# Performance work log

Hardware: AMD Instinct MI355X
Metric: run time of the kernel (lower is better)

The kernel has to match this reference:

```python
import jax, jax.numpy as jnp
import numpy as np

D_MODEL = 128
D_EDGE = 64


def setup_inputs() -> dict:
    key = jax.random.key(0)
    ks = jax.random.split(key, 12)
    B, N, E = 4, 50000, 600000
    x = jax.random.normal(ks[0], (B, N, D_MODEL), dtype=jnp.float32)
    edge_index = jax.random.randint(ks[1], (2, E), 0, N, dtype=jnp.int64)
    e_emb = jax.random.normal(ks[2], (E, D_EDGE), dtype=jnp.float32)
    batch_index = jax.random.randint(ks[3], (E,), 0, B, dtype=jnp.int64)
    s = 1.0 / np.sqrt(D_MODEL)
    se = 1.0 / np.sqrt(D_EDGE)
    Wq = jax.random.normal(ks[4], (D_MODEL, D_MODEL), dtype=jnp.float32) * s
    bq = jnp.zeros((D_MODEL,), dtype=jnp.float32)
    Wk = jax.random.normal(ks[5], (D_MODEL, D_MODEL), dtype=jnp.float32) * s
    bk = jnp.zeros((D_MODEL,), dtype=jnp.float32)
    Wv = jax.random.normal(ks[6], (D_MODEL, D_MODEL), dtype=jnp.float32) * s
    bv = jnp.zeros((D_MODEL,), dtype=jnp.float32)
    Wew = jax.random.normal(ks[7], (D_EDGE, D_MODEL), dtype=jnp.float32) * se
    bew = jnp.zeros((D_MODEL,), dtype=jnp.float32)
    Wev = jax.random.normal(ks[8], (D_EDGE, D_MODEL), dtype=jnp.float32) * se
    bev = jnp.zeros((D_MODEL,), dtype=jnp.float32)
    Wa = jax.random.normal(ks[9], (D_MODEL, 1), dtype=jnp.float32) * s
    return {"x": x, "edge_index": edge_index, "e_emb": e_emb,
            "batch_index": batch_index, "n_heads": 8,
            "Wq": Wq, "bq": bq, "Wk": Wk, "bk": bk, "Wv": Wv, "bv": bv,
            "Wew": Wew, "bew": bew, "Wev": Wev, "bev": bev, "Wa": Wa}


def reference(x, edge_index, e_emb, batch_index, n_heads,
              Wq, bq, Wk, bk, Wv, bv, Wew, bew, Wev, bev, Wa):
    B, N, d = x.shape
    d_h = d // n_heads
    Q = x @ Wq + bq          # [B, N, d]
    K = x @ Wk + bk
    V = x @ Wv + bv
    Ew = e_emb @ Wew + bew   # [E, d]
    Ev = e_emb @ Wev + bev
    src, dst = edge_index[0], edge_index[1]
    q_src = Q[batch_index, src, :]   # [E, d] gathers
    k_dst = K[batch_index, dst, :]
    v_dst = V[batch_index, dst, :]
    att_raw = q_src + k_dst + Ew
    att_logit = (att_raw @ Wa)[:, 0] / np.sqrt(d_h).astype(np.float32)
    att_exp = jnp.exp(att_logit)     # [E]
    group = batch_index * N + dst
    att_sum = jax.ops.segment_sum(att_exp, group, num_segments=B * N)
    alpha = att_exp / (att_sum[group] + 1e-9)
    msg = alpha[:, None] * (v_dst + Ev)          # [E, d]
    group_src = batch_index * N + src
    out_flat = jax.ops.segment_sum(msg, group_src, num_segments=B * N)
    return out_flat.reshape(B, N, d)
```

## Files before the change

### kernel.cpp

```cpp
#include <hip/hip_runtime.h>

#define DM 128
#define DE 64

static constexpr int kB = 4;
static constexpr int kN = 50000;
static constexpr int kE = 600000;
static constexpr int kNodes = kB * kN;

static constexpr size_t OFF_V    = 0;
static constexpr size_t OFF_T    = OFF_V + (size_t)kNodes * DM;
static constexpr size_t OFF_QA   = OFF_T + (size_t)kNodes * DE;
static constexpr size_t OFF_KA   = OFF_QA + kNodes;
static constexpr size_t OFF_ASUM = OFF_KA + kNodes;
static constexpr size_t OFF_CNT  = OFF_ASUM + kNodes;
static constexpr size_t OFF_AEXP = OFF_CNT + kNodes;
static constexpr size_t OFF_OFFS = OFF_AEXP + kE;
static constexpr size_t OFF_POS  = OFF_OFFS + kNodes;
static constexpr size_t OFF_BSUM = OFF_POS + kE;
static constexpr size_t OFF_BPRE = OFF_BSUM + 1024;
static constexpr size_t OFF_REC  = OFF_BPRE + 1024;
static constexpr size_t OFF_WQA  = OFF_REC + (size_t)kE * 4;
static constexpr size_t OFF_WKA  = OFF_WQA + DM;
static constexpr size_t OFF_WEWA = OFF_WKA + DM;
static constexpr size_t OFF_CB   = OFF_WEWA + DE;

static constexpr int kScanBlocks = (kNodes + 255) / 256;

__global__ void k0_combine(const float* __restrict__ Wq, const float* __restrict__ Wk,
                           const float* __restrict__ Wew, const float* __restrict__ Wa,
                           const float* __restrict__ bq, const float* __restrict__ bk,
                           const float* __restrict__ bew, float* __restrict__ ws) {
  int t = threadIdx.x;
  if (t < DM) {
    float a = 0.f;
    for (int j = 0; j < DM; ++j) a += Wq[t * DM + j] * Wa[j];
    ws[OFF_WQA + t] = a;
  } else if (t < 2 * DM) {
    int i = t - DM;
    float a = 0.f;
    for (int j = 0; j < DM; ++j) a += Wk[i * DM + j] * Wa[j];
    ws[OFF_WKA + i] = a;
  } else if (t < 2 * DM + DE) {
    int i = t - 2 * DM;
    float a = 0.f;
    for (int j = 0; j < DM; ++j) a += Wew[i * DM + j] * Wa[j];
    ws[OFF_WEWA + i] = a;
  }
  if (t == 0) {
    float a = 0.f;
    for (int j = 0; j < DM; ++j) a += (bq[j] + bk[j] + bew[j]) * Wa[j];
    ws[OFF_CB] = a;
  }
}

__global__ __launch_bounds__(256) void k1_node(const float* __restrict__ x,
                                               const float* __restrict__ Wv,
                                               const float* __restrict__ bv,
                                               float* __restrict__ ws) {
  __shared__ float xs[64][132];
  __shared__ float wvs[32][132];
  const int t = threadIdx.x;
  const int row0 = blockIdx.x * 64;

  const float4* xg = (const float4*)(x + (size_t)row0 * DM);
  #pragma unroll
  for (int i = 0; i < 8; ++i) {
    int idx = t + i * 256;
    int r = idx >> 5, c = (idx & 31) * 4;
    *(float4*)&xs[r][c] = xg[idx];
  }
  __syncthreads();

  if (t < 128) {
    const int r = t & 63;
    const float* wvec = (t < 64) ? (ws + OFF_WQA) : (ws + OFF_WKA);
    float a = 0.f;
    for (int k = 0; k < DM; k += 4) {
      a += xs[r][k] * wvec[k] + xs[r][k + 1] * wvec[k + 1] +
           xs[r][k + 2] * wvec[k + 2] + xs[r][k + 3] * wvec[k + 3];
    }
    float* dstp = (t < 64) ? (ws + OFF_QA) : (ws + OFF_KA);
    dstp[row0 + r] = a;
  }

  const int tx = t & 15, ty = t >> 4;
  const int j0 = tx * 8, r0 = ty * 4;
  float acc[4][8];
  #pragma unroll
  for (int i = 0; i < 4; ++i)
    #pragma unroll
    for (int j = 0; j < 8; ++j) acc[i][j] = 0.f;

  for (int kc = 0; kc < 4; ++kc) {
    __syncthreads();
    const float4* wg = (const float4*)(Wv + (size_t)kc * 32 * DM);
    #pragma unroll
    for (int i = 0; i < 4; ++i) {
      int idx = t + i * 256;
      int r = idx >> 5, c = (idx & 31) * 4;
      *(float4*)&wvs[r][c] = wg[idx];
    }
    __syncthreads();
    const int kb = kc * 32;
    #pragma unroll
    for (int kk = 0; kk < 32; kk += 4) {
      float xv[4][4];
      #pragma unroll
      for (int i = 0; i < 4; ++i) {
        float4 tmp = *(const float4*)&xs[r0 + i][kb + kk];
        xv[i][0] = tmp.x; xv[i][1] = tmp.y; xv[i][2] = tmp.z; xv[i][3] = tmp.w;
      }
      #pragma unroll
      for (int d = 0; d < 4; ++d) {
        float4 w0 = *(const float4*)&wvs[kk + d][j0];
        float4 w1 = *(const float4*)&wvs[kk + d][j0 + 4];
        float wj[8] = {w0.x, w0.y, w0.z, w0.w, w1.x, w1.y, w1.z, w1.w};
        #pragma unroll
        for (int i = 0; i < 4; ++i)
          #pragma unroll
          for (int j = 0; j < 8; ++j) acc[i][j] += xv[i][d] * wj[j];
      }
    }
  }

  const float4 bv0 = *(const float4*)&bv[j0];
  const float4 bv1 = *(const float4*)&bv[j0 + 4];
  float* Vp = ws + OFF_V + (size_t)row0 * DM;
  #pragma unroll
  for (int i = 0; i < 4; ++i) {
    float4 o0 = make_float4(acc[i][0] + bv0.x, acc[i][1] + bv0.y,
                            acc[i][2] + bv0.z, acc[i][3] + bv0.w);
    float4 o1 = make_float4(acc[i][4] + bv1.x, acc[i][5] + bv1.y,
                            acc[i][6] + bv1.z, acc[i][7] + bv1.w);
    *(float4*)&Vp[(size_t)(r0 + i) * DM + j0] = o0;
    *(float4*)&Vp[(size_t)(r0 + i) * DM + j0 + 4] = o1;
  }
}

__global__ __launch_bounds__(256) void k2_edge1(const int* __restrict__ ei,
                                                const int* __restrict__ bidx,
                                                const float* __restrict__ eemb,
                                                float* __restrict__ ws) {
  __shared__ float wewa_s[DE];
  __shared__ float cb_s;
  int t = threadIdx.x;
  if (t < DE) wewa_s[t] = ws[OFF_WEWA + t];
  if (t == DE) cb_s = ws[OFF_CB];
  __syncthreads();
  int e = blockIdx.x * 256 + t;
  if (e >= kE) return;
  int s = ei[e];
  int d = ei[kE + e];
  int b = bidx[e];
  const float4* emb = (const float4*)(eemb + (size_t)e * DE);
  float a = 0.f;
  #pragma unroll
  for (int i = 0; i < 16; ++i) {
    float4 v = emb[i];
    a += v.x * wewa_s[i * 4] + v.y * wewa_s[i * 4 + 1] +
         v.z * wewa_s[i * 4 + 2] + v.w * wewa_s[i * 4 + 3];
  }
  float logit = (ws[OFF_QA + b * kN + s] + ws[OFF_KA + b * kN + d] + a + cb_s) * 0.25f;
  float ex = __expf(logit);
  ws[OFF_AEXP + e] = ex;
  unsafeAtomicAdd(&ws[OFF_ASUM + b * kN + d], ex);
  int* wsi = (int*)ws;
  int gs = b * kN + s;
  wsi[OFF_POS + e] = atomicAdd(&wsi[OFF_CNT + gs], 1);
}

__global__ __launch_bounds__(256) void k_scan1(float* __restrict__ ws) {
  __shared__ int sh[256];
  int* wsi = (int*)ws;
  const int tid = threadIdx.x;
  const int i = blockIdx.x * 256 + tid;
  int v = (i < kNodes) ? wsi[OFF_CNT + i] : 0;
  int acc = v;
  sh[tid] = acc;
  __syncthreads();
  #pragma unroll
  for (int ofs = 1; ofs < 256; ofs <<= 1) {
    int add = (tid >= ofs) ? sh[tid - ofs] : 0;
    __syncthreads();
    acc += add;
    sh[tid] = acc;
    __syncthreads();
  }
  if (i < kNodes) wsi[OFF_OFFS + i] = acc - v;
  if (tid == 255) wsi[OFF_BSUM + blockIdx.x] = acc;
}

__global__ __launch_bounds__(1024) void k_scan2(float* __restrict__ ws) {
  __shared__ int sh[1024];
  int* wsi = (int*)ws;
  const int tid = threadIdx.x;
  int v = (tid < kScanBlocks) ? wsi[OFF_BSUM + tid] : 0;
  int acc = v;
  sh[tid] = acc;
  __syncthreads();
  for (int ofs = 1; ofs < 1024; ofs <<= 1) {
    int add = (tid >= ofs) ? sh[tid - ofs] : 0;
    __syncthreads();
    acc += add;
    sh[tid] = acc;
    __syncthreads();
  }
  wsi[OFF_BPRE + tid] = acc - v;
}

__global__ __launch_bounds__(256) void k_fill(const int* __restrict__ ei,
                                              const int* __restrict__ bidx,
                                              float* __restrict__ ws) {
  int e = blockIdx.x * 256 + threadIdx.x;
  if (e >= kE) return;
  int s = ei[e];
  int d = ei[kE + e];
  int b = bidx[e];
  int gs = b * kN + s;
  int gd = b * kN + d;
  const int* wsi = (const int*)ws;
  float alpha = ws[OFF_AEXP + e] / (ws[OFF_ASUM + gd] + 1e-9f);
  int p = wsi[OFF_OFFS + gs] + wsi[OFF_BPRE + (gs >> 8)] + wsi[OFF_POS + e];
  float4 r;
  r.x = alpha;
  r.y = __int_as_float(gd);
  r.z = __int_as_float(e);
  r.w = 0.f;
  ((float4*)(ws + OFF_REC))[p] = r;
}

__global__ __launch_bounds__(256) void k3_gather(const float* __restrict__ eemb,
                                                 const float* __restrict__ bev,
                                                 float* __restrict__ ws,
                                                 float* __restrict__ out) {
  const int lane = threadIdx.x & 63;
  const int g = (blockIdx.x * 256 + threadIdx.x) >> 6;
  if (g >= kNodes) return;
  const int* wsi = (const int*)ws;
  const float* V = ws + OFF_V;
  float* T = ws + OFF_T;
  const float4* rec = (const float4*)(ws + OFF_REC);
  const float bev0 = bev[lane];
  const float bev1 = bev[64 + lane];

  const int start = wsi[OFF_OFFS + g] + wsi[OFF_BPRE + (g >> 8)];
  const int deg = wsi[OFF_CNT + g];
  float o0 = 0.f, o1 = 0.f, tac = 0.f, ss = 0.f;
  for (int base = 0; base < deg; base += 4) {
    const int rem = deg - base;
    const int c1 = (rem > 1) ? 1 : 0;
    const int c2 = (rem > 2) ? 2 : c1;
    const int c3 = (rem > 3) ? 3 : c2;
    float4 r0 = rec[start + base];
    float4 r1 = rec[start + base + c1];
    float4 r2 = rec[start + base + c2];
    float4 r3 = rec[start + base + c3];
    float a0 = r0.x;
    float a1 = (rem > 1) ? r1.x : 0.f;
    float a2 = (rem > 2) ? r2.x : 0.f;
    float a3 = (rem > 3) ? r3.x : 0.f;
    const size_t gd0 = (size_t)__float_as_int(r0.y) * DM;
    const size_t gd1 = (size_t)__float_as_int(r1.y) * DM;
    const size_t gd2 = (size_t)__float_as_int(r2.y) * DM;
    const size_t gd3 = (size_t)__float_as_int(r3.y) * DM;
    const size_t e0 = (size_t)__float_as_int(r0.z) * DE;
    const size_t e1 = (size_t)__float_as_int(r1.z) * DE;
    const size_t e2 = (size_t)__float_as_int(r2.z) * DE;
    const size_t e3 = (size_t)__float_as_int(r3.z) * DE;
    float v00 = V[gd0 + lane],      v01 = V[gd1 + lane];
    float v02 = V[gd2 + lane],      v03 = V[gd3 + lane];
    float v10 = V[gd0 + 64 + lane], v11 = V[gd1 + 64 + lane];
    float v12 = V[gd2 + 64 + lane], v13 = V[gd3 + 64 + lane];
    float m0 = eemb[e0 + lane],     m1 = eemb[e1 + lane];
    float m2 = eemb[e2 + lane],     m3 = eemb[e3 + lane];
    o0 += a0 * v00 + a1 * v01 + a2 * v02 + a3 * v03;
    o1 += a0 * v10 + a1 * v11 + a2 * v12 + a3 * v13;
    tac += a0 * m0 + a1 * m1 + a2 * m2 + a3 * m3;
    ss += a0 + a1 + a2 + a3;
  }
  out[(size_t)g * DM + lane] = o0 + ss * bev0;
  out[(size_t)g * DM + 64 + lane] = o1 + ss * bev1;
  T[(size_t)g * DE + lane] = tac;
}

__global__ __launch_bounds__(256) void k4_wev(const float* __restrict__ Wev,
                                              float* __restrict__ ws,
                                              float* __restrict__ out) {
  __shared__ float ts[64][68];
  __shared__ float wes[64][132];
  const int t = threadIdx.x;
  const int row0 = blockIdx.x * 64;
  const float* T = ws + OFF_T;

  const float4* tg = (const float4*)(T + (size_t)row0 * DE);
  #pragma unroll
  for (int i = 0; i < 4; ++i) {
    int idx = t + i * 256;
    int r = idx >> 4, c = (idx & 15) * 4;
    *(float4*)&ts[r][c] = tg[idx];
  }
  const float4* wg = (const float4*)Wev;
  #pragma unroll
  for (int i = 0; i < 8; ++i) {
    int idx = t + i * 256;
    int r = idx >> 5, c = (idx & 31) * 4;
    *(float4*)&wes[r][c] = wg[idx];
  }
  __syncthreads();

  const int tx = t & 15, ty = t >> 4;
  const int j0 = tx * 8, r0 = ty * 4;
  float acc[4][8];
  #pragma unroll
  for (int i = 0; i < 4; ++i)
    #pragma unroll
    for (int j = 0; j < 8; ++j) acc[i][j] = 0.f;

  #pragma unroll
  for (int kk = 0; kk < DE; kk += 4) {
    float xv[4][4];
    #pragma unroll
    for (int i = 0; i < 4; ++i) {
      float4 tmp = *(const float4*)&ts[r0 + i][kk];
      xv[i][0] = tmp.x; xv[i][1] = tmp.y; xv[i][2] = tmp.z; xv[i][3] = tmp.w;
    }
    #pragma unroll
    for (int d = 0; d < 4; ++d) {
      float4 w0 = *(const float4*)&wes[kk + d][j0];
      float4 w1 = *(const float4*)&wes[kk + d][j0 + 4];
      float wj[8] = {w0.x, w0.y, w0.z, w0.w, w1.x, w1.y, w1.z, w1.w};
      #pragma unroll
      for (int i = 0; i < 4; ++i)
        #pragma unroll
        for (int j = 0; j < 8; ++j) acc[i][j] += xv[i][d] * wj[j];
    }
  }

  #pragma unroll
  for (int i = 0; i < 4; ++i) {
    size_t g = (size_t)(row0 + r0 + i);
    float4 o0 = *(const float4*)&out[g * DM + j0];
    float4 o1 = *(const float4*)&out[g * DM + j0 + 4];
    o0.x += acc[i][0]; o0.y += acc[i][1]; o0.z += acc[i][2]; o0.w += acc[i][3];
    o1.x += acc[i][4]; o1.y += acc[i][5]; o1.z += acc[i][6]; o1.w += acc[i][7];
    *(float4*)&out[g * DM + j0] = o0;
    *(float4*)&out[g * DM + j0 + 4] = o1;
  }
}

extern "C" void kernel_launch(void* const* d_in, const int* in_sizes, int n_in,
                              void* d_out, int out_size, void* d_ws, size_t ws_size,
                              hipStream_t stream) {
  const float* x    = (const float*)d_in[0];
  const int*   ei   = (const int*)d_in[1];
  const float* eemb = (const float*)d_in[2];
  const int*   bidx = (const int*)d_in[3];
  const float* Wq  = (const float*)d_in[5];
  const float* bq  = (const float*)d_in[6];
  const float* Wk  = (const float*)d_in[7];
  const float* bk  = (const float*)d_in[8];
  const float* Wv  = (const float*)d_in[9];
  const float* bv  = (const float*)d_in[10];
  const float* Wew = (const float*)d_in[11];
  const float* bew = (const float*)d_in[12];
  const float* Wev = (const float*)d_in[13];
  const float* bev = (const float*)d_in[14];
  const float* Wa  = (const float*)d_in[15];
  float* ws  = (float*)d_ws;
  float* out = (float*)d_out;

  hipMemsetAsync(ws + OFF_ASUM, 0, (size_t)2 * kNodes * sizeof(float), stream);

  k0_combine<<<1, 320, 0, stream>>>(Wq, Wk, Wew, Wa, bq, bk, bew, ws);
  k1_node<<<kNodes / 64, 256, 0, stream>>>(x, Wv, bv, ws);
  k2_edge1<<<(kE + 255) / 256, 256, 0, stream>>>(ei, bidx, eemb, ws);
  k_scan1<<<kScanBlocks, 256, 0, stream>>>(ws);
  k_scan2<<<1, 1024, 0, stream>>>(ws);
  k_fill<<<(kE + 255) / 256, 256, 0, stream>>>(ei, bidx, ws);
  k3_gather<<<kNodes / 4, 256, 0, stream>>>(eemb, bev, ws, out);
  k4_wev<<<kNodes / 64, 256, 0, stream>>>(Wev, ws, out);
}
```

Before: 633.9 us.

## Compute V projection with split-bf16 MFMA instead of FP32 FMA tiles

Replaces the FP32 SIMT GEMM for V = x@Wv with bf16x3-style MFMA (hi*hi + hi*lo + lo*hi) on 128-row tiles with swizzled LDS layouts. A new pre-kernel splits Wv into hi/lo bf16 halves in a permuted layout. This aims to cut the compute cost of the node projection while keeping near-FP32 accuracy, at the cost of an extra launch, 128KB LDS per block (lower occupancy), and scalar non-vectorized V stores.

```diff
diff --git a/kernel.cpp b/kernel.cpp
--- a/kernel.cpp
+++ b/kernel.cpp
@@ -24,8 +24,24 @@
 static constexpr size_t OFF_WKA  = OFF_WQA + DM;
 static constexpr size_t OFF_WEWA = OFF_WKA + DM;
 static constexpr size_t OFF_CB   = OFF_WEWA + DE;
+static constexpr size_t OFF_WTH  = OFF_CB + 4;
+static constexpr size_t OFF_WTL  = OFF_WTH + 8192;
 
 static constexpr int kScanBlocks = (kNodes + 255) / 256;
+
+typedef __attribute__((ext_vector_type(8))) short s8;
+typedef __attribute__((ext_vector_type(4))) float f4;
+
+__device__ inline void split2(float f, unsigned short& h, unsigned short& lo) {
+  unsigned u = __float_as_uint(f);
+  unsigned r = u + 0x7FFFu + ((u >> 16) & 1u);
+  h = (unsigned short)(r >> 16);
+  float fh = __uint_as_float((unsigned)h << 16);
+  float d = f - fh;
+  unsigned u2 = __float_as_uint(d);
+  unsigned r2 = u2 + 0x7FFFu + ((u2 >> 16) & 1u);
+  lo = (unsigned short)(r2 >> 16);
+}
 
 __global__ void k0_combine(const float* __restrict__ Wq, const float* __restrict__ Wk,
                            const float* __restrict__ Wew, const float* __restrict__ Wa,
@@ -54,87 +70,131 @@
   }
 }
 
-__global__ __launch_bounds__(256) void k1_node(const float* __restrict__ x,
-                                               const float* __restrict__ Wv,
+__global__ __launch_bounds__(256) void k0b_wsplit(const float* __restrict__ Wv,
+                                                  float* __restrict__ ws) {
+  int idx = blockIdx.x * 256 + threadIdx.x;
+  int j = idx & 127, k = idx >> 7;
+  float w = Wv[k * DM + j];
+  unsigned short hi, lo;
+  split2(w, hi, lo);
+  int kc = k & 31;
+  int kp = (k & ~31) | (((kc >> 2) & 3) << 3) | ((kc >> 4) << 2) | (kc & 3);
+  ((short*)(ws + OFF_WTH))[j * 128 + kp] = (short)hi;
+  ((short*)(ws + OFF_WTL))[j * 128 + kp] = (short)lo;
+}
+
+__global__ __launch_bounds__(512) void k1_node(const float* __restrict__ x,
                                                const float* __restrict__ bv,
                                                float* __restrict__ ws) {
-  __shared__ float xs[64][132];
-  __shared__ float wvs[32][132];
+  __shared__ short xh[128][128];
+  __shared__ short xl[128][128];
+  __shared__ short wh[128][128];
+  __shared__ short wl[128][128];
   const int t = threadIdx.x;
-  const int row0 = blockIdx.x * 64;
-
-  const float4* xg = (const float4*)(x + (size_t)row0 * DM);
+  const int row0 = blockIdx.x * 128;
+
+  const short* wtgh = (const short*)(ws + OFF_WTH);
+  const short* wtgl = (const short*)(ws + OFF_WTL);
+  #pragma unroll
+  for (int i = 0; i < 4; ++i) {
+    int idx = t + i * 512;
+    int j = idx >> 4;
+    int c8 = (idx & 15) * 8;
+    int col = (((c8 >> 3) ^ (j & 7)) << 3);
+    *(int4*)&wh[j][col] = *(const int4*)(wtgh + j * 128 + c8);
+    *(int4*)&wl[j][col] = *(const int4*)(wtgl + j * 128 + c8);
+  }
+
   #pragma unroll
   for (int i = 0; i < 8; ++i) {
-    int idx = t + i * 256;
-    int r = idx >> 5, c = (idx & 31) * 4;
-    *(float4*)&xs[r][c] = xg[idx];
-  }
+    int idx = t + i * 512;
+    int r = idx >> 5;
+    int c4 = (idx & 31) * 4;
+    int rg = row0 + r; if (rg > kNodes - 1) rg = kNodes - 1;
+    float4 v = *(const float4*)(x + (size_t)rg * DM + c4);
+    unsigned short h0, h1, h2, h3, l0, l1, l2, l3;
+    split2(v.x, h0, l0); split2(v.y, h1, l1);
+    split2(v.z, h2, l2); split2(v.w, h3, l3);
+    int kc = c4 & 31;
+    int cp = (c4 & ~31) | (((kc >> 2) & 3) << 3) | ((kc >> 4) << 2);
+    int col = ((((cp >> 3) ^ (r & 7)) << 3)) | (cp & 7);
+    *(short4*)&xh[r][col] = make_short4((short)h0, (short)h1, (short)h2, (short)h3);
+    *(short4*)&xl[r][col] = make_short4((short)l0, (short)l1, (short)l2, (short)l3);
+  }
+
+  if (t < 256) {
+    int r = t & 127;
+    int rg = row0 + r;
+    if (rg < kNodes) {
+      const float* wvec = (t < 128) ? (ws + OFF_WQA) : (ws + OFF_WKA);
+      const float* xr = x + (size_t)rg * DM;
+      float a = 0.f;
+      #pragma unroll
+      for (int k = 0; k < DM; k += 4) {
+        float4 xv = *(const float4*)(xr + k);
+        float4 wv = *(const float4*)(wvec + k);
+        a += xv.x * wv.x + xv.y * wv.y + xv.z * wv.z + xv.w * wv.w;
+      }
+      ((t < 128) ? (ws + OFF_QA) : (ws + OFF_KA))[rg] = a;
+    }
+  }
+
   __syncthreads();
 
-  if (t < 128) {
-    const int r = t & 63;
-    const float* wvec = (t < 64) ? (ws + OFF_WQA) : (ws + OFF_WKA);
-    float a = 0.f;
-    for (int k = 0; k < DM; k += 4) {
-      a += xs[r][k] * wvec[k] + xs[r][k + 1] * wvec[k + 1] +
-           xs[r][k + 2] * wvec[k + 2] + xs[r][k + 3] * wvec[k + 3];
-    }
-    float* dstp = (t < 64) ? (ws + OFF_QA) : (ws + OFF_KA);
-    dstp[row0 + r] = a;
-  }
-
-  const int tx = t & 15, ty = t >> 4;
-  const int j0 = tx * 8, r0 = ty * 4;
-  float acc[4][8];
-  #pragma unroll
-  for (int i = 0; i < 4; ++i)
-    #pragma unroll
-    for (int j = 0; j < 8; ++j) acc[i][j] = 0.f;
-
-  for (int kc = 0; kc < 4; ++kc) {
-    __syncthreads();
-    const float4* wg = (const float4*)(Wv + (size_t)kc * 32 * DM);
-    #pragma unroll
-    for (int i = 0; i < 4; ++i) {
-      int idx = t + i * 256;
-      int r = idx >> 5, c = (idx & 31) * 4;
-      *(float4*)&wvs[r][c] = wg[idx];
-    }
-    __syncthreads();
-    const int kb = kc * 32;
-    #pragma unroll
-    for (int kk = 0; kk < 32; kk += 4) {
-      float xv[4][4];
+  const int l = t & 63;
+  const int wid = t >> 6;
+  const int wr = wid >> 1;
+  const int wc = wid & 1;
+  const int lrow = l & 15;
+  const int lg = l >> 4;
+
+  f4 acc[2][4];
+  #pragma unroll
+  for (int i = 0; i < 2; ++i)
+    #pragma unroll
+    for (int j = 0; j < 4; ++j) acc[i][j] = (f4){0.f, 0.f, 0.f, 0.f};
+
+  #pragma unroll
+  for (int ks = 0; ks < 4; ++ks) {
+    s8 ah[2], al[2], bh[4], bl[4];
+    #pragma unroll
+    for (int i = 0; i < 2; ++i) {
+      int r = wr * 32 + i * 16 + lrow;
+      int col = (((ks * 4 + lg) ^ (r & 7)) << 3);
+      ah[i] = *(const s8*)&xh[r][col];
+      al[i] = *(const s8*)&xl[r][col];
+    }
+    #pragma unroll
+    for (int j = 0; j < 4; ++j) {
+      int r = wc * 64 + j * 16 + lrow;
+      int col = (((ks * 4 + lg) ^ (r & 7)) << 3);
+      bh[j] = *(const s8*)&wh[r][col];
+      bl[j] = *(const s8*)&wl[r][col];
+    }
+    #pragma unroll
+    for (int i = 0; i < 2; ++i)
       #pragma unroll
-      for (int i = 0; i < 4; ++i) {
-        float4 tmp = *(const float4*)&xs[r0 + i][kb + kk];
-        xv[i][0] = tmp.x; xv[i][1] = tmp.y; xv[i][2] = tmp.z; xv[i][3] = tmp.w;
+      for (int j = 0; j < 4; ++j) {
+        acc[i][j] = __builtin_amdgcn_mfma_f32_16x16x32_bf16(ah[i], bh[j], acc[i][j], 0, 0, 0);
+        acc[i][j] = __builtin_amdgcn_mfma_f32_16x16x32_bf16(ah[i], bl[j], acc[i][j], 0, 0, 0);
+        acc[i][j] = __builtin_amdgcn_mfma_f32_16x16x32_bf16(al[i], bh[j], acc[i][j], 0, 0, 0);
       }
+  }
+
+  float* V = ws + OFF_V;
+  #pragma unroll
+  for (int i = 0; i < 2; ++i) {
+    int rb = row0 + wr * 32 + i * 16 + lg * 4;
+    #pragma unroll
+    for (int j = 0; j < 4; ++j) {
+      int colj = wc * 64 + j * 16 + lrow;
+      float bvv = bv[colj];
       #pragma unroll
-      for (int d = 0; d < 4; ++d) {
-        float4 w0 = *(const float4*)&wvs[kk + d][j0];
-        float4 w1 = *(const float4*)&wvs[kk + d][j0 + 4];
-        float wj[8] = {w0.x, w0.y, w0.z, w0.w, w1.x, w1.y, w1.z, w1.w};
-        #pragma unroll
-        for (int i = 0; i < 4; ++i)
-          #pragma unroll
-          for (int j = 0; j < 8; ++j) acc[i][j] += xv[i][d] * wj[j];
+      for (int q = 0; q < 4; ++q) {
+        int rr = rb + q;
+        if (rr < kNodes) V[(size_t)rr * DM + colj] = acc[i][j][q] + bvv;
       }
     }
-  }
-
-  const float4 bv0 = *(const float4*)&bv[j0];
-  const float4 bv1 = *(const float4*)&bv[j0 + 4];
-  float* Vp = ws + OFF_V + (size_t)row0 * DM;
-  #pragma unroll
-  for (int i = 0; i < 4; ++i) {
-    float4 o0 = make_float4(acc[i][0] + bv0.x, acc[i][1] + bv0.y,
-                            acc[i][2] + bv0.z, acc[i][3] + bv0.w);
-    float4 o1 = make_float4(acc[i][4] + bv1.x, acc[i][5] + bv1.y,
-                            acc[i][6] + bv1.z, acc[i][7] + bv1.w);
-    *(float4*)&Vp[(size_t)(r0 + i) * DM + j0] = o0;
-    *(float4*)&Vp[(size_t)(r0 + i) * DM + j0 + 4] = o1;
   }
 }
 
@@ -373,7 +433,8 @@
   hipMemsetAsync(ws + OFF_ASUM, 0, (size_t)2 * kNodes * sizeof(float), stream);
 
   k0_combine<<<1, 320, 0, stream>>>(Wq, Wk, Wew, Wa, bq, bk, bew, ws);
-  k1_node<<<kNodes / 64, 256, 0, stream>>>(x, Wv, bv, ws);
+  k0b_wsplit<<<64, 256, 0, stream>>>(Wv, ws);
+  k1_node<<<(kNodes + 127) / 128, 512, 0, stream>>>(x, bv, ws);
   k2_edge1<<<(kE + 255) / 256, 256, 0, stream>>>(ei, bidx, eemb, ws);
   k_scan1<<<kScanBlocks, 256, 0, stream>>>(ws);
   k_scan2<<<1, 1024, 0, stream>>>(ws);
```

New measurement: 639.6 us. Within noise of the previous version (+0.9%).
